# Performance work log

Hardware: AMD Instinct MI355X
Metric: run time of the kernel (lower is better)

Reference implementation:

```python
import jax, jax.numpy as jnp
import numpy as np

KH, KW = 3, 3
PAD, STRIDE = 1, 1
KD = 3  # depth kernel extent; extended with one zero slice -> 4 indices


def _unfold(x, pad, stride):
    # x: (B, C, H, W) -> (B, C, KH*KW, oH, oW), patches ordered row-major like F.unfold
    B, C, H, W = x.shape
    xp = jnp.pad(x, ((0, 0), (0, 0), (pad, pad), (pad, pad)))
    oH = (H + 2 * pad - KH) // stride + 1
    oW = (W + 2 * pad - KW) // stride + 1
    pats = [xp[:, :, i:i + (oH - 1) * stride + 1:stride, j:j + (oW - 1) * stride + 1:stride]
            for i in range(KH) for j in range(KW)]
    return jnp.stack(pats, axis=2)


def setup_inputs() -> dict:
    key = jax.random.key(0)
    k1, k2, k3 = jax.random.split(key, 3)
    features = jax.random.normal(k1, (4, 16, 512, 512), dtype=jnp.float32)
    depth = jax.random.randint(k2, (4, 512, 512), 0, 8, dtype=jnp.int32)
    weight = jax.random.normal(k3, (32, 16, 3, 3, 3), dtype=jnp.float32) * 0.05
    return {"features": features, "depth": depth, "weight": weight}


def reference(features, depth, weight):
    oC, iC = weight.shape[0], weight.shape[1]
    # unfolded input patches: (B, iC, 9, oH, oW)
    patches = _unfold(features, PAD, STRIDE)
    # unfolded depth: (B, 9, oH, oW); padding fills with depth 0 (matches F.unfold)
    dpat = _unfold(depth[:, None, :, :].astype(jnp.int32), PAD, STRIDE)[:, 0]
    center = dpat[:, KH * KW // 2][:, None]  # (B, 1, oH, oW)
    diff = dpat - center
    # diff < -1 or diff >= 1 -> select appended zero slice (index 3); else diff+1
    idx = jnp.where((diff < -1) | (diff >= 1), 3, diff + 1)  # (B, 9, oH, oW) in [0, 3]
    onehot = jax.nn.one_hot(idx, KD + 1, dtype=features.dtype)  # (B, 9, oH, oW, 4)
    # extended weight with zero depth-slice: (oC, iC, 4, 9)
    ext_w = jnp.concatenate([weight, jnp.zeros_like(weight[:, :, :1])], axis=2)
    ext_w = ext_w.reshape(oC, iC, KD + 1, KH * KW)
    # per-pixel depth-gated 3x3x3 conv (bias is never added in the original op)
    out = jnp.einsum('oidk,bkhwd,bikhw->bohw', ext_w, onehot, patches)
    return out
```

## Files before the change

### kernel.cpp

```cpp
#include <hip/hip_runtime.h>
#include <hip/hip_bf16.h>


#define IC 16
#define OC 32
#define Hh 512
#define Ww 512
#define HW (Hh * Ww)
#define TW 256
#define TR 4
#define PXS 20
#define SENT (1 << 20)
#define NT 4

typedef __attribute__((ext_vector_type(8))) short short8;
typedef __attribute__((ext_vector_type(4))) float float4v;
typedef __attribute__((ext_vector_type(2))) unsigned int uint2v;

__device__ __forceinline__ unsigned short f2bf(float x) {
    unsigned u = __float_as_uint(x);
    unsigned r = u + 0x7FFFu + ((u >> 16) & 1u);
    return (unsigned short)(r >> 16);
}

__device__ __forceinline__ unsigned packbf(float a, float b) {
    union { __hip_bfloat162 h2; unsigned u; } cv;
    cv.h2 = __float22bfloat162_rn(make_float2(a, b));
    return cv.u;
}

__global__ void prep_weights(const float* __restrict__ wgt,
                             unsigned short* __restrict__ wsA) {
    int e = blockIdx.x * 256 + threadIdx.x;
    if (e >= 9 * 2 * 64 * 8) return;
    int j    = e & 7;
    int lane = (e >> 3) & 63;
    int mt   = (e >> 9) & 1;
    int c    = e >> 10;
    int oc = mt * 16 + (lane & 15);
    int kk = ((lane >> 4) << 3) + j;
    wsA[e] = f2bf(wgt[oc * 432 + (kk >> 1) * 27 + (kk & 1) * 9 + c]);
}

__global__ __launch_bounds__(512, 1) void depconv_fused(
    const float* __restrict__ feat,
    const int*   __restrict__ depth,
    const unsigned short* __restrict__ wsA,
    float*       __restrict__ out)
{
    __shared__ unsigned short ftile[2][6][TW + 2][PXS];
    __shared__ int            dtile[2][6][TW + 2];

    const int tid = threadIdx.x;
    const int bid = blockIdx.x;
    const int wg = (bid & 7) * 32 + (bid >> 3);
    const int t0 = wg * NT;

    const int h8 = tid >> 8;
    const int xl = tid & 255;

    const int lane = tid & 63;
    const int wv   = tid >> 6;
    const int g    = lane >> 4;
    const int n    = lane & 15;
    const int rr   = wv >> 1;
    const int xoff = (wv & 1) * 128;
    const int q    = lane >> 4;
    const int oc0  = lane & 15;

    short8 wfrag[9][2];
    {
        const short8* ap = (const short8*)wsA;
#pragma unroll
        for (int c = 0; c < 9; ++c) {
            wfrag[c][0] = ap[(c * 2 + 0) * 64 + lane];
            wfrag[c][1] = ap[(c * 2 + 1) * 64 + lane];
        }
    }

    float pf[6][8];
    int   pd[6];

    auto issue = [&](int tt) {
        const int b      = tt >> 8;
        const int h0     = ((tt >> 1) & 127) * TR;
        const int wstart = (tt & 1) * TW;
        const int x   = wstart - 1 + xl;
        const bool xin = (unsigned)x < (unsigned)Ww;
        const int xc  = x < 0 ? 0 : (x > Ww - 1 ? Ww - 1 : x);
        const float* fb  = feat + (size_t)(b * IC + 8 * h8) * HW + xc;
        const int*   dbp = depth + (b << 18) + xc;
#pragma unroll
        for (int r = 0; r < 6; ++r) {
            const int y = h0 - 1 + r;
            const bool yin = (unsigned)y < (unsigned)Hh;
            const int yc = y < 0 ? 0 : (y > Hh - 1 ? Hh - 1 : y);
            const float* fpl = fb + (size_t)yc * Ww;
            if (h8 == 0) pd[r] = (yin & xin) ? dbp[yc * Ww] : SENT;
#pragma unroll
            for (int i = 0; i < 8; ++i)
                pf[r][i] = fpl[(size_t)i * HW];
        }
    };

    auto write_tile = [&](int p, int tt) {
        const int b      = tt >> 8;
        const int h0     = ((tt >> 1) & 127) * TR;
        const int wstart = (tt & 1) * TW;
#pragma unroll
        for (int r = 0; r < 6; ++r) {
            if (h8 == 0) dtile[p][r][xl] = pd[r];
            unsigned short* wp = &ftile[p][r][xl][h8 * 8];
            *(uint2v*)wp       = (uint2v){packbf(pf[r][0], pf[r][1]),
                                          packbf(pf[r][2], pf[r][3])};
            *(uint2v*)(wp + 4) = (uint2v){packbf(pf[r][4], pf[r][5]),
                                          packbf(pf[r][6], pf[r][7])};
        }
        if (xl < 2) {
            const int xt = wstart - 1 + 256 + xl;
            const bool xtin = (unsigned)xt < (unsigned)Ww;
            const int xct = xt > Ww - 1 ? Ww - 1 : xt;
            const float* fb  = feat + (size_t)(b * IC + 8 * h8) * HW + xct;
            const int*   dbp = depth + (b << 18) + xct;
#pragma unroll
            for (int r = 0; r < 6; ++r) {
                const int y = h0 - 1 + r;
                const bool yin = (unsigned)y < (unsigned)Hh;
                const int yc = y < 0 ? 0 : (y > Hh - 1 ? Hh - 1 : y);
                const float* fpl = fb + (size_t)yc * Ww;
                if (h8 == 0)
                    dtile[p][r][256 + xl] = (yin & xtin) ? dbp[yc * Ww] : SENT;
                unsigned short* wq = &ftile[p][r][256 + xl][h8 * 8];
                *(uint2v*)wq       = (uint2v){packbf(fpl[0],              fpl[(size_t)1 * HW]),
                                              packbf(fpl[(size_t)2 * HW], fpl[(size_t)3 * HW])};
                *(uint2v*)(wq + 4) = (uint2v){packbf(fpl[(size_t)4 * HW], fpl[(size_t)5 * HW]),
                                              packbf(fpl[(size_t)6 * HW], fpl[(size_t)7 * HW])};
            }
        }
    };

    auto compute = [&](int p, int tt) {
        const int b      = tt >> 8;
        const int h0     = ((tt >> 1) & 127) * TR;
        const int wstart = (tt & 1) * TW;
        const int h = h0 + rr;
        float* opb0 = out + ((size_t)(b * OC + oc0) << 18) + (size_t)h * Ww;
        for (int it = 0; it < 8; ++it) {
            const int xb = xoff + it * 16 + n;
            const int dc = dtile[p][rr + 1][xb + 1];
            float4v acc0 = {0.f, 0.f, 0.f, 0.f};
            float4v acc1 = {0.f, 0.f, 0.f, 0.f};
#pragma unroll
            for (int t = 0; t < 9; ++t) {
                const int kh = t / 3, kw = t % 3;
                unsigned mm;
                if (t == 4) {
                    mm = 0xffff0000u;
                } else {
                    const int diff = dtile[p][rr + kh][xb + kw] - dc;
                    mm = (diff == 0) ? 0xffff0000u : ((diff == -1) ? 0x0000ffffu : 0u);
                }
                const uint2v pr = *(const uint2v*)(&ftile[p][rr + kh][xb + kw][g << 2]);
                union { short8 s; unsigned u[4]; } bf;
                bf.u[0] = __builtin_amdgcn_perm(0u, pr.x, 0x01000100u) & mm;
                bf.u[1] = __builtin_amdgcn_perm(0u, pr.x, 0x03020302u) & mm;
                bf.u[2] = __builtin_amdgcn_perm(0u, pr.y, 0x01000100u) & mm;
                bf.u[3] = __builtin_amdgcn_perm(0u, pr.y, 0x03020302u) & mm;

                acc0 = __builtin_amdgcn_mfma_f32_16x16x32_bf16(bf.s, wfrag[t][0], acc0, 0, 0, 0);
                acc1 = __builtin_amdgcn_mfma_f32_16x16x32_bf16(bf.s, wfrag[t][1], acc1, 0, 0, 0);
            }
            const int w16 = wstart + xoff + it * 16;
            float* op = opb0 + (w16 + 4 * q);
            *(float4v*)op                     = acc0;
            *(float4v*)(op + (size_t)16 * HW) = acc1;
        }
    };

    issue(t0);
    write_tile(0, t0);
    __syncthreads();
#pragma unroll 1
    for (int i = 0; i < NT; ++i) {
        const int p = i & 1;
        if (i + 1 < NT) issue(t0 + i + 1);
        compute(p, t0 + i);
        if (i + 1 < NT) {
            write_tile(p ^ 1, t0 + i + 1);
            __syncthreads();
        }
    }
}

extern "C" void kernel_launch(void* const* d_in, const int* in_sizes, int n_in,
                              void* d_out, int out_size, void* d_ws, size_t ws_size,
                              hipStream_t stream) {
    const float* feat  = (const float*)d_in[0];
    const int*   depth = (const int*)d_in[1];
    const float* wgt   = (const float*)d_in[2];
    float* out = (float*)d_out;

    unsigned short* wsA = (unsigned short*)d_ws;

    prep_weights<<<36, 256, 0, stream>>>(wgt, wsA);
    depconv_fused<<<256, 512, 0, stream>>>(feat, depth, wsA, out);
}
```

Measured before the change: 216.7 us.

## Split block into dedicated producer and consumer waves for tile staging

Grows the block from 512 to 768 threads. The four extra waves only load and convert the next tile into shared memory, while the original eight waves only run the MFMA compute. Before, every thread prefetched into registers and then wrote to shared memory itself. With dedicated producers each loading all 16 channels per column, consumer waves no longer hold prefetch registers, and the two roles can overlap. The cost is fewer loader threads doing more loads each, plus a sync every iteration.

```diff
diff --git a/kernel.cpp b/kernel.cpp
--- a/kernel.cpp
+++ b/kernel.cpp
@@ -42,7 +42,7 @@
     wsA[e] = f2bf(wgt[oc * 432 + (kk >> 1) * 27 + (kk & 1) * 9 + c]);
 }
 
-__global__ __launch_bounds__(512, 1) void depconv_fused(
+__global__ __launch_bounds__(768, 1) void depconv_fused(
     const float* __restrict__ feat,
     const int*   __restrict__ depth,
     const unsigned short* __restrict__ wsA,
@@ -56,8 +56,8 @@
     const int wg = (bid & 7) * 32 + (bid >> 3);
     const int t0 = wg * NT;
 
-    const int h8 = tid >> 8;
-    const int xl = tid & 255;
+    const bool isProd = (tid >= 512);
+    const int  xl     = tid - 512;
 
     const int lane = tid & 63;
     const int wv   = tid >> 6;
@@ -69,7 +69,7 @@
     const int oc0  = lane & 15;
 
     short8 wfrag[9][2];
-    {
+    if (!isProd) {
         const short8* ap = (const short8*)wsA;
 #pragma unroll
         for (int c = 0; c < 9; ++c) {
@@ -78,17 +78,14 @@
         }
     }
 
-    float pf[6][8];
-    int   pd[6];
-
-    auto issue = [&](int tt) {
+    auto stage = [&](int p, int tt) {
         const int b      = tt >> 8;
         const int h0     = ((tt >> 1) & 127) * TR;
         const int wstart = (tt & 1) * TW;
         const int x   = wstart - 1 + xl;
         const bool xin = (unsigned)x < (unsigned)Ww;
         const int xc  = x < 0 ? 0 : (x > Ww - 1 ? Ww - 1 : x);
-        const float* fb  = feat + (size_t)(b * IC + 8 * h8) * HW + xc;
+        const float* fb  = feat + (size_t)b * IC * HW + xc;
         const int*   dbp = depth + (b << 18) + xc;
 #pragma unroll
         for (int r = 0; r < 6; ++r) {
@@ -96,46 +93,41 @@
             const bool yin = (unsigned)y < (unsigned)Hh;
             const int yc = y < 0 ? 0 : (y > Hh - 1 ? Hh - 1 : y);
             const float* fpl = fb + (size_t)yc * Ww;
-            if (h8 == 0) pd[r] = (yin & xin) ? dbp[yc * Ww] : SENT;
+            dtile[p][r][xl] = (yin & xin) ? dbp[yc * Ww] : SENT;
+            unsigned pk[8];
 #pragma unroll
             for (int i = 0; i < 8; ++i)
-                pf[r][i] = fpl[(size_t)i * HW];
+                pk[i] = packbf(fpl[(size_t)(2 * i) * HW],
+                               fpl[(size_t)(2 * i + 1) * HW]);
+            unsigned short* wp = &ftile[p][r][xl][0];
+            *(uint2v*)(wp)      = (uint2v){pk[0], pk[1]};
+            *(uint2v*)(wp + 4)  = (uint2v){pk[2], pk[3]};
+            *(uint2v*)(wp + 8)  = (uint2v){pk[4], pk[5]};
+            *(uint2v*)(wp + 12) = (uint2v){pk[6], pk[7]};
         }
-    };
-
-    auto write_tile = [&](int p, int tt) {
-        const int b      = tt >> 8;
-        const int h0     = ((tt >> 1) & 127) * TR;
-        const int wstart = (tt & 1) * TW;
-#pragma unroll
-        for (int r = 0; r < 6; ++r) {
-            if (h8 == 0) dtile[p][r][xl] = pd[r];
-            unsigned short* wp = &ftile[p][r][xl][h8 * 8];
-            *(uint2v*)wp       = (uint2v){packbf(pf[r][0], pf[r][1]),
-                                          packbf(pf[r][2], pf[r][3])};
-            *(uint2v*)(wp + 4) = (uint2v){packbf(pf[r][4], pf[r][5]),
-                                          packbf(pf[r][6], pf[r][7])};
-        }
-        if (xl < 2) {
-            const int xt = wstart - 1 + 256 + xl;
+        const int ti = xl - 128;
+        if ((unsigned)ti < 12u) {
+            const int r  = ti >> 1;
+            const int tp = ti & 1;
+            const int xt = wstart - 1 + 256 + tp;
             const bool xtin = (unsigned)xt < (unsigned)Ww;
             const int xct = xt > Ww - 1 ? Ww - 1 : xt;
-            const float* fb  = feat + (size_t)(b * IC + 8 * h8) * HW + xct;
-            const int*   dbp = depth + (b << 18) + xct;
+            const int y = h0 - 1 + r;
+            const bool yin = (unsigned)y < (unsigned)Hh;
+            const int yc = y < 0 ? 0 : (y > Hh - 1 ? Hh - 1 : y);
+            const float* fpl = feat + (size_t)b * IC * HW + (size_t)yc * Ww + xct;
+            dtile[p][r][256 + tp] = (yin & xtin) ? depth[(b << 18) + yc * Ww + xct]
+                                                 : SENT;
+            unsigned qk[8];
 #pragma unroll
-            for (int r = 0; r < 6; ++r) {
-                const int y = h0 - 1 + r;
-                const bool yin = (unsigned)y < (unsigned)Hh;
-                const int yc = y < 0 ? 0 : (y > Hh - 1 ? Hh - 1 : y);
-                const float* fpl = fb + (size_t)yc * Ww;
-                if (h8 == 0)
-                    dtile[p][r][256 + xl] = (yin & xtin) ? dbp[yc * Ww] : SENT;
-                unsigned short* wq = &ftile[p][r][256 + xl][h8 * 8];
-                *(uint2v*)wq       = (uint2v){packbf(fpl[0],              fpl[(size_t)1 * HW]),
-                                              packbf(fpl[(size_t)2 * HW], fpl[(size_t)3 * HW])};
-                *(uint2v*)(wq + 4) = (uint2v){packbf(fpl[(size_t)4 * HW], fpl[(size_t)5 * HW]),
-                                              packbf(fpl[(size_t)6 * HW], fpl[(size_t)7 * HW])};
-            }
+            for (int i = 0; i < 8; ++i)
+                qk[i] = packbf(fpl[(size_t)(2 * i) * HW],
+                               fpl[(size_t)(2 * i + 1) * HW]);
+            unsigned short* wq = &ftile[p][r][256 + tp][0];
+            *(uint2v*)(wq)      = (uint2v){qk[0], qk[1]};
+            *(uint2v*)(wq + 4)  = (uint2v){qk[2], qk[3]};
+            *(uint2v*)(wq + 8)  = (uint2v){qk[4], qk[5]};
+            *(uint2v*)(wq + 12) = (uint2v){qk[6], qk[7]};
         }
     };
 
@@ -145,6 +137,7 @@
         const int wstart = (tt & 1) * TW;
         const int h = h0 + rr;
         float* opb0 = out + ((size_t)(b * OC + oc0) << 18) + (size_t)h * Ww;
+#pragma unroll 1
         for (int it = 0; it < 8; ++it) {
             const int xb = xoff + it * 16 + n;
             const int dc = dtile[p][rr + 1][xb + 1];
@@ -177,18 +170,16 @@
         }
     };
 
-    issue(t0);
-    write_tile(0, t0);
+    if (isProd) stage(0, t0);
     __syncthreads();
 #pragma unroll 1
     for (int i = 0; i < NT; ++i) {
-        const int p = i & 1;
-        if (i + 1 < NT) issue(t0 + i + 1);
-        compute(p, t0 + i);
-        if (i + 1 < NT) {
-            write_tile(p ^ 1, t0 + i + 1);
-            __syncthreads();
+        if (!isProd) {
+            compute(i & 1, t0 + i);
+        } else if (i + 1 < NT) {
+            stage((i + 1) & 1, t0 + i + 1);
         }
+        __syncthreads();
     }
 }
 
@@ -203,5 +194,5 @@
     unsigned short* wsA = (unsigned short*)d_ws;
 
     prep_weights<<<36, 256, 0, stream>>>(wgt, wsA);
-    depconv_fused<<<256, 512, 0, stream>>>(feat, depth, wsA, out);
+    depconv_fused<<<256, 768, 0, stream>>>(feat, depth, wsA, out);
 }
```

New measurement: 209.5 us, median of 3. -3.3%, faster.

## Pre-pack features to padded bf16 channel-last and stage tiles via async global-to-LDS loads

Applied to the files above, without the earlier changes.

Two new pre-passes run before the convolution. One converts features to a zero-border-padded, channel-last bf16 buffer with an XOR swizzle of the channel groups. The other writes a padded 16-bit depth map that holds a sentinel value at the borders. The main kernel then copies tiles straight into LDS with global_load_lds, which drops the per-element strided fp32 loads, the bf16 conversion and the boundary clamping from the hot loop. Tile height shrinks to 2 rows, the grid doubles and two blocks per CU are targeted to raise occupancy. The cost is an extra read of the features plus a bf16 write and re-read, and the border cells of the packed buffer are never written; they rely on the depth mask to zero their contribution.

```diff
diff --git a/kernel.cpp b/kernel.cpp
--- a/kernel.cpp
+++ b/kernel.cpp
@@ -8,25 +8,38 @@
 #define Ww 512
 #define HW (Hh * Ww)
 #define TW 256
-#define TR 4
-#define PXS 20
-#define SENT (1 << 20)
+#define TR 2
 #define NT 4
+#define SENTu 0x1000
+#define PY  514
+#define PXF 514
+#define PXD 516
+#define FTP_BYTES (4ull * PY * PXF * IC * 2)
 
 typedef __attribute__((ext_vector_type(8))) short short8;
 typedef __attribute__((ext_vector_type(4))) float float4v;
 typedef __attribute__((ext_vector_type(2))) unsigned int uint2v;
+typedef __attribute__((ext_vector_type(4))) unsigned int uint4v;
 
 __device__ __forceinline__ unsigned short f2bf(float x) {
     unsigned u = __float_as_uint(x);
     unsigned r = u + 0x7FFFu + ((u >> 16) & 1u);
     return (unsigned short)(r >> 16);
 }
-
 __device__ __forceinline__ unsigned packbf(float a, float b) {
     union { __hip_bfloat162 h2; unsigned u; } cv;
     cv.h2 = __float22bfloat162_rn(make_float2(a, b));
     return cv.u;
+}
+__device__ __forceinline__ void gl16(const void* g, void* l) {
+    __builtin_amdgcn_global_load_lds(
+        (const __attribute__((address_space(1))) unsigned int*)g,
+        (__attribute__((address_space(3))) unsigned int*)l, 16, 0, 0);
+}
+__device__ __forceinline__ void gl4(const void* g, void* l) {
+    __builtin_amdgcn_global_load_lds(
+        (const __attribute__((address_space(1))) unsigned int*)g,
+        (__attribute__((address_space(3))) unsigned int*)l, 4, 0, 0);
 }
 
 __global__ void prep_weights(const float* __restrict__ wgt,
@@ -42,30 +55,71 @@
     wsA[e] = f2bf(wgt[oc * 432 + (kk >> 1) * 27 + (kk & 1) * 9 + c]);
 }
 
-__global__ __launch_bounds__(512, 1) void depconv_fused(
-    const float* __restrict__ feat,
-    const int*   __restrict__ depth,
+__global__ __launch_bounds__(256) void prep_feat(const float* __restrict__ feat,
+                                                 unsigned short* __restrict__ ftp) {
+    const int e  = blockIdx.x * 256 + threadIdx.x;
+    const int xq = e & 127;
+    const int y  = (e >> 7) & 511;
+    const int b  = e >> 16;
+    float4v v[16];
+    const float* fb = feat + ((size_t)(b * IC) << 18) + (y << 9) + (xq << 2);
+#pragma unroll
+    for (int ic = 0; ic < IC; ++ic)
+        v[ic] = *(const float4v*)(fb + ((size_t)ic << 18));
+#pragma unroll
+    for (int i = 0; i < 4; ++i) {
+        const int xp = (xq << 2) + i + 1;
+        const int q  = (xp >> 2) & 3;
+        unsigned pk[8];
+#pragma unroll
+        for (int j = 0; j < 8; ++j)
+            pk[j] = packbf(v[2 * j][i], v[2 * j + 1][i]);
+        uint2v c0 = {pk[0], pk[1]}, c1 = {pk[2], pk[3]},
+               c2 = {pk[4], pk[5]}, c3 = {pk[6], pk[7]};
+        if (q & 1) { uint2v t = c0; c0 = c1; c1 = t; t = c2; c2 = c3; c3 = t; }
+        if (q & 2) { uint2v t = c0; c0 = c2; c2 = t; t = c1; c1 = c3; c3 = t; }
+        uint4v* dst = (uint4v*)(ftp + (((size_t)b * PY + (y + 1)) * PXF + xp) * 16);
+        dst[0] = (uint4v){c0.x, c0.y, c1.x, c1.y};
+        dst[1] = (uint4v){c2.x, c2.y, c3.x, c3.y};
+    }
+}
+
+__global__ __launch_bounds__(256) void prep_depth(const int* __restrict__ depth,
+                                                  unsigned short* __restrict__ dpad) {
+    const int e = blockIdx.x * 256 + threadIdx.x;
+    if (e >= 4 * PY * PXD) return;
+    const int xp = e % PXD;
+    const int yb = e / PXD;
+    const int yp = yb % PY;
+    const int b  = yb / PY;
+    unsigned short v = (unsigned short)SENTu;
+    const int xi = xp - 1, yi = yp - 1;
+    if ((unsigned)xi < (unsigned)Ww && (unsigned)yi < (unsigned)Hh)
+        v = (unsigned short)depth[(b << 18) + (yi << 9) + xi];
+    dpad[e] = v;
+}
+
+__global__ __launch_bounds__(512, 2) void depconv_main(
+    const unsigned short* __restrict__ ftp,
+    const unsigned short* __restrict__ dpad,
     const unsigned short* __restrict__ wsA,
-    float*       __restrict__ out)
+    float* __restrict__ out)
 {
-    __shared__ unsigned short ftile[2][6][TW + 2][PXS];
-    __shared__ int            dtile[2][6][TW + 2];
+    __shared__ alignas(16) unsigned short ftile[2][TR + 2][258][16];
+    __shared__ alignas(16) unsigned short dtile[2][TR + 2][260];
 
     const int tid = threadIdx.x;
     const int bid = blockIdx.x;
-    const int wg = (bid & 7) * 32 + (bid >> 3);
-    const int t0 = wg * NT;
-
-    const int h8 = tid >> 8;
-    const int xl = tid & 255;
+    const int wg  = (bid & 7) * 64 + (bid >> 3);
+    const int t0  = wg * NT;
 
     const int lane = tid & 63;
     const int wv   = tid >> 6;
     const int g    = lane >> 4;
     const int n    = lane & 15;
-    const int rr   = wv >> 1;
-    const int xoff = (wv & 1) * 128;
-    const int q    = lane >> 4;
+    const int rr   = wv >> 2;
+    const int xoff = (wv & 3) * 64;
+    const int qs   = lane >> 4;
     const int oc0  = lane & 15;
 
     short8 wfrag[9][2];
@@ -78,89 +132,57 @@
         }
     }
 
-    float pf[6][8];
-    int   pd[6];
-
-    auto issue = [&](int tt) {
-        const int b      = tt >> 8;
-        const int h0     = ((tt >> 1) & 127) * TR;
-        const int wstart = (tt & 1) * TW;
-        const int x   = wstart - 1 + xl;
-        const bool xin = (unsigned)x < (unsigned)Ww;
-        const int xc  = x < 0 ? 0 : (x > Ww - 1 ? Ww - 1 : x);
-        const float* fb  = feat + (size_t)(b * IC + 8 * h8) * HW + xc;
-        const int*   dbp = depth + (b << 18) + xc;
-#pragma unroll
-        for (int r = 0; r < 6; ++r) {
-            const int y = h0 - 1 + r;
-            const bool yin = (unsigned)y < (unsigned)Hh;
-            const int yc = y < 0 ? 0 : (y > Hh - 1 ? Hh - 1 : y);
-            const float* fpl = fb + (size_t)yc * Ww;
-            if (h8 == 0) pd[r] = (yin & xin) ? dbp[yc * Ww] : SENT;
-#pragma unroll
-            for (int i = 0; i < 8; ++i)
-                pf[r][i] = fpl[(size_t)i * HW];
+    auto stageF = [&](int p, int tt) {
+        const int b = tt >> 9, rowblk = (tt >> 1) & 255, colblk = tt & 1;
+        const int h0 = rowblk * TR, wstart = colblk * TW;
+        const char* gbase = (const char*)(ftp + (((size_t)b * PY + h0) * PXF + wstart) * 16);
+#pragma unroll
+        for (int r = 0; r < TR + 2; ++r) {
+            const char* rg = gbase + (size_t)r * (PXF * 32);
+            char* lr = (char*)&ftile[p][r][0][0];
+            gl16(rg + tid * 16,      lr + wv * 1024);
+            gl16(rg + 64 + tid * 16, lr + 64 + wv * 1024);
         }
     };
-
-    auto write_tile = [&](int p, int tt) {
-        const int b      = tt >> 8;
-        const int h0     = ((tt >> 1) & 127) * TR;
-        const int wstart = (tt & 1) * TW;
-#pragma unroll
-        for (int r = 0; r < 6; ++r) {
-            if (h8 == 0) dtile[p][r][xl] = pd[r];
-            unsigned short* wp = &ftile[p][r][xl][h8 * 8];
-            *(uint2v*)wp       = (uint2v){packbf(pf[r][0], pf[r][1]),
-                                          packbf(pf[r][2], pf[r][3])};
-            *(uint2v*)(wp + 4) = (uint2v){packbf(pf[r][4], pf[r][5]),
-                                          packbf(pf[r][6], pf[r][7])};
-        }
-        if (xl < 2) {
-            const int xt = wstart - 1 + 256 + xl;
-            const bool xtin = (unsigned)xt < (unsigned)Ww;
-            const int xct = xt > Ww - 1 ? Ww - 1 : xt;
-            const float* fb  = feat + (size_t)(b * IC + 8 * h8) * HW + xct;
-            const int*   dbp = depth + (b << 18) + xct;
-#pragma unroll
-            for (int r = 0; r < 6; ++r) {
-                const int y = h0 - 1 + r;
-                const bool yin = (unsigned)y < (unsigned)Hh;
-                const int yc = y < 0 ? 0 : (y > Hh - 1 ? Hh - 1 : y);
-                const float* fpl = fb + (size_t)yc * Ww;
-                if (h8 == 0)
-                    dtile[p][r][256 + xl] = (yin & xtin) ? dbp[yc * Ww] : SENT;
-                unsigned short* wq = &ftile[p][r][256 + xl][h8 * 8];
-                *(uint2v*)wq       = (uint2v){packbf(fpl[0],              fpl[(size_t)1 * HW]),
-                                              packbf(fpl[(size_t)2 * HW], fpl[(size_t)3 * HW])};
-                *(uint2v*)(wq + 4) = (uint2v){packbf(fpl[(size_t)4 * HW], fpl[(size_t)5 * HW]),
-                                              packbf(fpl[(size_t)6 * HW], fpl[(size_t)7 * HW])};
-            }
+    auto stageD = [&](int p, int tt) {
+        const int b = tt >> 9, rowblk = (tt >> 1) & 255, colblk = tt & 1;
+        const int h0 = rowblk * TR, wstart = colblk * TW;
+        const char* gb = (const char*)(dpad + ((size_t)b * PY + h0) * PXD + wstart);
+        char* lb = (char*)&dtile[p][0][0];
+#pragma unroll
+        for (int pass = 0; pass < 2; ++pass) {
+            const unsigned off = pass ? 32u : 0u;
+            const unsigned d   = off + tid * 4;
+            const unsigned row = d / 520u;
+            const unsigned col = d - row * 520u;
+            gl4(gb + (size_t)row * (PXD * 2) + col, lb + off + wv * 256);
         }
     };
 
     auto compute = [&](int p, int tt) {
-        const int b      = tt >> 8;
-        const int h0     = ((tt >> 1) & 127) * TR;
-        const int wstart = (tt & 1) * TW;
+        const int b = tt >> 9, rowblk = (tt >> 1) & 255, colblk = tt & 1;
+        const int h0 = rowblk * TR, wstart = colblk * TW;
         const int h = h0 + rr;
-        float* opb0 = out + ((size_t)(b * OC + oc0) << 18) + (size_t)h * Ww;
-        for (int it = 0; it < 8; ++it) {
+        float* opb0 = out + ((size_t)(b * OC + oc0) << 18) + ((size_t)h << 9);
+#pragma unroll 1
+        for (int it = 0; it < 4; ++it) {
             const int xb = xoff + it * 16 + n;
-            const int dc = dtile[p][rr + 1][xb + 1];
+            const int dc = (int)dtile[p][rr + 1][xb + 1];
             float4v acc0 = {0.f, 0.f, 0.f, 0.f};
             float4v acc1 = {0.f, 0.f, 0.f, 0.f};
 #pragma unroll
             for (int t = 0; t < 9; ++t) {
                 const int kh = t / 3, kw = t % 3;
+                const int px = xb + kw;
                 unsigned mm;
                 if (t == 4) {
                     mm = 0xffff0000u;
                 } else {
-                    const int diff = dtile[p][rr + kh][xb + kw] - dc;
+                    const int diff = (int)dtile[p][rr + kh][px] - dc;
                     mm = (diff == 0) ? 0xffff0000u : ((diff == -1) ? 0x0000ffffu : 0u);
                 }
-                const uint2v pr = *(const uint2v*)(&ftile[p][rr + kh][xb + kw][g << 2]);
+                const int slot = (g ^ ((px >> 2) & 3)) << 2;
+                const uint2v pr = *(const uint2v*)(&ftile[p][rr + kh][px][slot]);
                 union { short8 s; unsigned u[4]; } bf;
                 bf.u[0] = __builtin_amdgcn_perm(0u, pr.x, 0x01000100u) & mm;
                 bf.u[1] = __builtin_amdgcn_perm(0u, pr.x, 0x03020302u) & mm;
@@ -171,24 +193,24 @@
                 acc1 = __builtin_amdgcn_mfma_f32_16x16x32_bf16(bf.s, wfrag[t][1], acc1, 0, 0, 0);
             }
             const int w16 = wstart + xoff + it * 16;
-            float* op = opb0 + (w16 + 4 * q);
-            *(float4v*)op                     = acc0;
-            *(float4v*)(op + (size_t)16 * HW) = acc1;
+            float* op = opb0 + (w16 + 4 * qs);
+            *(float4v*)op                      = acc0;
+            *(float4v*)(op + ((size_t)16 << 18)) = acc1;
         }
     };
 
-    issue(t0);
-    write_tile(0, t0);
+    stageF(0, t0);
+    stageD(0, t0);
     __syncthreads();
 #pragma unroll 1
     for (int i = 0; i < NT; ++i) {
         const int p = i & 1;
-        if (i + 1 < NT) issue(t0 + i + 1);
+        if (i + 1 < NT) {
+            stageF(p ^ 1, t0 + i + 1);
+            stageD(p ^ 1, t0 + i + 1);
+        }
         compute(p, t0 + i);
-        if (i + 1 < NT) {
-            write_tile(p ^ 1, t0 + i + 1);
-            __syncthreads();
-        }
+        __syncthreads();
     }
 }
 
@@ -200,8 +222,12 @@
     const float* wgt   = (const float*)d_in[2];
     float* out = (float*)d_out;
 
-    unsigned short* wsA = (unsigned short*)d_ws;
+    unsigned short* wsA  = (unsigned short*)d_ws;
+    unsigned short* ftp  = (unsigned short*)((char*)d_ws + 32768);
+    unsigned short* dpad = (unsigned short*)((char*)d_ws + 32768 + FTP_BYTES);
 
     prep_weights<<<36, 256, 0, stream>>>(wgt, wsA);
-    depconv_fused<<<256, 512, 0, stream>>>(feat, depth, wsA, out);
-}
+    prep_feat<<<1024, 256, 0, stream>>>(feat, ftp);
+    prep_depth<<<(4 * PY * PXD + 255) / 256, 256, 0, stream>>>(depth, dpad);
+    depconv_main<<<512, 512, 0, stream>>>(ftp, dpad, wsA, out);
+}
```

New measurement: 256.3 us. +18.3%, slower.
